# Optimization experiments

Measured on AMD Instinct MI355X. Metric: run time of the kernel, lower is better.

## Reference

```python
import jax, jax.numpy as jnp
import numpy as np

N = 50000   # nodes
R = 4       # relation groups
E = 800000  # nnz per relation adjacency
ED = 200000 # decoded edges
H = 128     # hidden_dim
L = 64      # latent_dim
DH = 64     # decoder_hidden_dim


def setup_inputs() -> dict:
    key = jax.random.key(0)
    ks = iter(jax.random.split(key, 64))
    def nrm(shape, scale=1.0):
        return jax.random.normal(next(ks), shape, dtype=jnp.float32) * scale
    inp = {}
    inp["x_process"] = nrm((N, 62))
    inp["x_file"] = nrm((N, 37))
    inp["x_network"] = nrm((N, 37))
    def lin(prefix, din, dout):
        s = 1.0 / np.sqrt(din)
        inp[prefix + "_Ws"] = nrm((dout, din), s)
        inp[prefix + "_bs"] = nrm((dout,), s)
        inp[prefix + "_Wr"] = nrm((R, dout, din), s)
        inp[prefix + "_br"] = nrm((R, dout), s)
    lin("p1", 62, H); lin("p2", H, L)
    lin("f1", 37, H); lin("f2", H, L)
    lin("n1", 37, H); lin("n2", H, L)
    inp["gate_W"] = nrm((3, L), 1.0 / np.sqrt(L))
    inp["gate_b"] = nrm((3,), 0.1)
    inp["dec_W1"] = nrm((DH, 4 * L), 1.0 / np.sqrt(4 * L))
    inp["dec_b1"] = nrm((DH,), 0.1)
    inp["dec_W2"] = nrm((1, DH), 1.0 / np.sqrt(DH))
    inp["dec_b2"] = nrm((1,), 0.1)
    inp["adj_rows"] = jax.random.randint(next(ks), (R, E), 0, N, dtype=jnp.int32)
    inp["adj_cols"] = jax.random.randint(next(ks), (R, E), 0, N, dtype=jnp.int32)
    inp["adj_vals"] = jax.random.uniform(next(ks), (R, E), dtype=jnp.float32) * 0.1
    inp["edge_src"] = jax.random.randint(next(ks), (ED,), 0, N, dtype=jnp.int32)
    inp["edge_dst"] = jax.random.randint(next(ks), (ED,), 0, N, dtype=jnp.int32)
    return inp


def reference(x_process, x_file, x_network,
              p1_Ws, p1_bs, p1_Wr, p1_br, p2_Ws, p2_bs, p2_Wr, p2_br,
              f1_Ws, f1_bs, f1_Wr, f1_br, f2_Ws, f2_bs, f2_Wr, f2_br,
              n1_Ws, n1_bs, n1_Wr, n1_br, n2_Ws, n2_bs, n2_Wr, n2_br,
              gate_W, gate_b, dec_W1, dec_b1, dec_W2, dec_b2,
              adj_rows, adj_cols, adj_vals, edge_src, edge_dst):
    def spmm(rows, cols, vals, x):  # A @ x, A in COO: out[row] += val * x[col]
        return jax.ops.segment_sum(vals[:, None] * x[cols], rows, num_segments=N)

    def rgcn_layer(x, Ws, bs, Wr, br):
        out = x @ Ws.T + bs  # self_linear
        for r in range(R):
            out = out + spmm(adj_rows[r], adj_cols[r], adj_vals[r], x) @ Wr[r].T + br[r]
        return out / float(R + 1)

    def encoder(x, W1s, b1s, W1r, b1r, W2s, b2s, W2r, b2r):
        h = jax.nn.relu(rgcn_layer(x, W1s, b1s, W1r, b1r))
        # dropout p=0.0 / eval mode -> identity
        return rgcn_layer(h, W2s, b2s, W2r, b2r)

    z_p = encoder(x_process, p1_Ws, p1_bs, p1_Wr, p1_br, p2_Ws, p2_bs, p2_Wr, p2_br)
    z_f = encoder(x_file, f1_Ws, f1_bs, f1_Wr, f1_br, f2_Ws, f2_bs, f2_Wr, f2_br)
    z_n = encoder(x_network, n1_Ws, n1_bs, n1_Wr, n1_br, n2_Ws, n2_bs, n2_Wr, n2_br)

    # gated multi-view fusion: three Linear(latent,1) gates -> softmax over views
    scores = jnp.stack([z_p @ gate_W[0] + gate_b[0],
                        z_f @ gate_W[1] + gate_b[1],
                        z_n @ gate_W[2] + gate_b[2]], axis=1)  # [N, 3]
    alpha = jax.nn.softmax(scores, axis=1)
    z = alpha[:, 0:1] * z_p + alpha[:, 1:2] * z_f + alpha[:, 2:3] * z_n  # [N, L]

    # mlp edge decoder
    zs = z[edge_src]
    zd = z[edge_dst]
    feats = jnp.concatenate([zs, zd, zs * zd, jnp.abs(zs - zd)], axis=1)  # [ED, 4L]
    hid = jax.nn.relu(feats @ dec_W1.T + dec_b1)
    logits = (hid @ dec_W2.T + dec_b2)[:, 0]  # [ED]
    return logits
```

## Files before the change

kernel.cpp:

```cpp
#include <hip/hip_runtime.h>

#define N_NODES 50000
#define R_REL   4
#define E_NNZ   800000
#define ED_EDGES 200000
#define H_DIM   128
#define L_DIM   64

#define RN_TOTAL (R_REL * N_NODES)
#define ETOT     (R_REL * E_NNZ)

#define EPB   8192
#define NB    391
#define RBK   196
#define KBK   (R_REL * RBK)
#define HTOT  (KBK * NB)
#define SCB   300
#define MAXB  6144

#define WS_RP    0u
#define WS_HIST  800256u
#define WS_BSUM  2026496u
#define WS_BIAS3 (WS_BSUM + 2048u)
#define WS_CV    2030592u
#define WS_TMP   27630720u
#define WS_XALL  53230720u
#define WS_SP    72430720u
#define WS_SF    122030720u
#define WS_SN    151630720u
#define WS_HPR   181230720u
#define WS_HN    WS_TMP
#define WS_HF    WS_SP
#define WS_YSP   WS_XALL
#define WS_YSF   (WS_SP + 25600000u)
#define WS_YRP   WS_SF
#define WS_YRF   WS_SN
#define WS_YSN   WS_HPR
#define WS_YRN   WS_HF
#define WS_Z     194030720u
#define WS_PART  WS_TMP

__device__ __forceinline__ ushort f2bf(float f) {
    unsigned u = __float_as_uint(f);
    unsigned r = (u + 0x7fffu + ((u >> 16) & 1u)) >> 16;
    return (ushort)r;
}
__device__ __forceinline__ float bf2f(ushort u) {
    return __uint_as_float(((unsigned)u) << 16);
}

__global__ void cast_xall_kernel(const float* __restrict__ xp, const float* __restrict__ xf,
                                 const float* __restrict__ xn, ushort* __restrict__ xall) {
    int i = blockIdx.x * 256 + threadIdx.x;
    if (i >= N_NODES * 192) return;
    int node = i / 192, k = i - node * 192;
    float v = 0.f;
    if (k < 62) v = xp[node * 62 + k];
    else if (k >= 64 && k < 138) {
        int j = k - 64, d = j >> 1;
        v = (j & 1) ? xn[node * 37 + d] : xf[node * 37 + d];
    }
    xall[i] = f2bf(v);
}

__global__ void radix_hist_kernel(const int* __restrict__ rows, int* __restrict__ H) {
    __shared__ int hist[KBK];
    int blk = blockIdx.x, t = threadIdx.x;
    for (int i = t; i < KBK; i += 256) hist[i] = 0;
    __syncthreads();
    int base = blk * EPB;
    #pragma unroll 1
    for (int i = 0; i < EPB / 256; i++) {
        int g = base + i * 256 + t;
        if (g < ETOT) {
            int r = g / E_NNZ;
            atomicAdd(&hist[r * RBK + (rows[g] >> 8)], 1);
        }
    }
    __syncthreads();
    for (int i = t; i < KBK; i += 256) H[i * NB + blk] = hist[i];
}

__global__ void scan_part_kernel(const int* __restrict__ H, int* __restrict__ bsum) {
    __shared__ int red[256];
    int base = blockIdx.x * 1024, t = threadIdx.x;
    int s = 0;
    #pragma unroll
    for (int i = 0; i < 4; i++) {
        int idx = base + i * 256 + t;
        if (idx < HTOT) s += H[idx];
    }
    red[t] = s; __syncthreads();
    for (int d = 128; d > 0; d >>= 1) {
        if (t < d) red[t] += red[t + d];
        __syncthreads();
    }
    if (t == 0) bsum[blockIdx.x] = red[0];
}

__global__ void scan_bsum_kernel(int* __restrict__ bsum, int* __restrict__ rp) {
    __shared__ int sh[512];
    int t = threadIdx.x;
    int v = (t < SCB) ? bsum[t] : 0;
    sh[t] = v; __syncthreads();
    for (int d = 1; d < 512; d <<= 1) {
        int u = (t >= d) ? sh[t - d] : 0;
        __syncthreads();
        sh[t] += u;
        __syncthreads();
    }
    if (t < SCB) bsum[t] = sh[t] - v;
    if (t == 0) rp[RN_TOTAL] = ETOT;
}

__global__ void scan_final_kernel(int* __restrict__ H, const int* __restrict__ bsum) {
    __shared__ int sh[256];
    int base = blockIdx.x * 1024, t = threadIdx.x;
    int c[4]; int s = 0;
    #pragma unroll
    for (int i = 0; i < 4; i++) {
        int idx = base + t * 4 + i;
        c[i] = (idx < HTOT) ? H[idx] : 0;
        s += c[i];
    }
    sh[t] = s; __syncthreads();
    for (int d = 1; d < 256; d <<= 1) {
        int u = (t >= d) ? sh[t - d] : 0;
        __syncthreads();
        sh[t] += u;
        __syncthreads();
    }
    int off = bsum[blockIdx.x] + sh[t] - s;
    #pragma unroll
    for (int i = 0; i < 4; i++) {
        int idx = base + t * 4 + i;
        if (idx < HTOT) H[idx] = off;
        off += c[i];
    }
}

__global__ void radix_scatter_kernel(const int* __restrict__ rows, const int* __restrict__ cols,
                                     const float* __restrict__ vals, const int* __restrict__ H,
                                     int2* __restrict__ tmp) {
    __shared__ int cur[KBK];
    int blk = blockIdx.x, t = threadIdx.x;
    for (int i = t; i < KBK; i += 256) cur[i] = H[i * NB + blk];
    __syncthreads();
    int base = blk * EPB;
    #pragma unroll 1
    for (int i = 0; i < EPB / 256; i++) {
        int g = base + i * 256 + t;
        if (g < ETOT) {
            int r = g / E_NNZ;
            int row = rows[g];
            int b = r * RBK + (row >> 8);
            int p = atomicAdd(&cur[b], 1);
            tmp[p] = make_int2(cols[g] | ((row & 255) << 16), __float_as_int(vals[g]));
        }
    }
}

__launch_bounds__(256)
__global__ void bucket_sort_kernel(const int2* __restrict__ tmp, const int* __restrict__ H,
                                   int* __restrict__ rp, int2* __restrict__ cse) {
    __shared__ int hist[256];
    __shared__ int sc[256];
    __shared__ int cur[256];
    __shared__ int2 eb[MAXB];
    int b = blockIdx.x, t = threadIdx.x;
    int start = H[b * NB];
    int end = (b == KBK - 1) ? ETOT : H[(b + 1) * NB];
    int cnt = end - start;
    bool useLds = (cnt <= MAXB);
    hist[t] = 0;
    __syncthreads();
    for (int i = t; i < cnt; i += 256) {
        int2 e = tmp[start + i];
        if (useLds) eb[i] = e;
        atomicAdd(&hist[(e.x >> 16) & 255], 1);
    }
    __syncthreads();
    sc[t] = hist[t]; __syncthreads();
    for (int d = 1; d < 256; d <<= 1) {
        int v = (t >= d) ? sc[t - d] : 0;
        __syncthreads();
        sc[t] += v;
        __syncthreads();
    }
    int pref = sc[t] - hist[t];
    int r = b / RBK, rh = b - r * RBK;
    int grow = rh * 256 + t;
    if (grow < N_NODES) rp[r * N_NODES + grow] = start + pref;
    cur[t] = start + pref;
    __syncthreads();
    for (int i = t; i < cnt; i += 256) {
        int2 e = useLds ? eb[i] : tmp[start + i];
        int rl = (e.x >> 16) & 255;
        int p = atomicAdd(&cur[rl], 1);
        cse[p] = make_int2(e.x & 0xFFFF, e.y);
    }
}

__global__ void spmm1_all_kernel(const ushort* __restrict__ xall,
                                 const int* __restrict__ rp, const int2* __restrict__ cse,
                                 float* __restrict__ Sp, float* __restrict__ Sf,
                                 float* __restrict__ Sn) {
    int wave = threadIdx.x >> 6, lane = threadIdx.x & 63;
    int row = blockIdx.x * 4 + wave;
    if (row >= N_NODES) return;
    int h = lane >> 5, j = lane & 31;
    unsigned d0 = 2u * (unsigned)j;
    unsigned po = d0;
    unsigned fo = 64u + 2u * d0;
    for (int r = 0; r < R_REL; r++) {
        int e0 = rp[r * N_NODES + row], e1 = rp[r * N_NODES + row + 1];
        float ap0 = 0.f, ap1 = 0.f, af0 = 0.f, af1 = 0.f, an0 = 0.f, an1 = 0.f;
        int e = e0;
        for (; e + 8 <= e1; e += 8) {
            int2 qA = cse[e + h],     qB = cse[e + 2 + h];
            int2 qC = cse[e + 4 + h], qD = cse[e + 6 + h];
            unsigned bA = (unsigned)qA.x * 192u, bB = (unsigned)qB.x * 192u;
            unsigned bC = (unsigned)qC.x * 192u, bD = (unsigned)qD.x * 192u;
            ushort2 pA = *(const ushort2*)(xall + bA + po);
            ushort2 pB = *(const ushort2*)(xall + bB + po);
            ushort2 pC = *(const ushort2*)(xall + bC + po);
            ushort2 pD = *(const ushort2*)(xall + bD + po);
            ushort4 uA = *(const ushort4*)(xall + bA + fo);
            ushort4 uB = *(const ushort4*)(xall + bB + fo);
            ushort4 uC = *(const ushort4*)(xall + bC + fo);
            ushort4 uD = *(const ushort4*)(xall + bD + fo);
            float vA = __int_as_float(qA.y), vB = __int_as_float(qB.y);
            float vC = __int_as_float(qC.y), vD = __int_as_float(qD.y);
            ap0 += vA * bf2f(pA.x) + vB * bf2f(pB.x) + vC * bf2f(pC.x) + vD * bf2f(pD.x);
            ap1 += vA * bf2f(pA.y) + vB * bf2f(pB.y) + vC * bf2f(pC.y) + vD * bf2f(pD.y);
            af0 += vA * bf2f(uA.x) + vB * bf2f(uB.x) + vC * bf2f(uC.x) + vD * bf2f(uD.x);
            an0 += vA * bf2f(uA.y) + vB * bf2f(uB.y) + vC * bf2f(uC.y) + vD * bf2f(uD.y);
            af1 += vA * bf2f(uA.z) + vB * bf2f(uB.z) + vC * bf2f(uC.z) + vD * bf2f(uD.z);
            an1 += vA * bf2f(uA.w) + vB * bf2f(uB.w) + vC * bf2f(uC.w) + vD * bf2f(uD.w);
        }
        for (; e < e1; e += 2) {
            int idx = e + h;
            int2 q = cse[idx < e1 ? idx : e1 - 1];
            float v = (idx < e1) ? __int_as_float(q.y) : 0.f;
            unsigned b = (unsigned)q.x * 192u;
            ushort2 p = *(const ushort2*)(xall + b + po);
            ushort4 u = *(const ushort4*)(xall + b + fo);
            ap0 += v * bf2f(p.x); ap1 += v * bf2f(p.y);
            af0 += v * bf2f(u.x); an0 += v * bf2f(u.y);
            af1 += v * bf2f(u.z); an1 += v * bf2f(u.w);
        }
        ap0 += __shfl_xor(ap0, 32); ap1 += __shfl_xor(ap1, 32);
        af0 += __shfl_xor(af0, 32); af1 += __shfl_xor(af1, 32);
        an0 += __shfl_xor(an0, 32); an1 += __shfl_xor(an1, 32);
        if (h == 0) {
            int d = (int)d0;
            if (d < 62) *(float2*)(Sp + row * 248 + r * 62 + d) = make_float2(ap0, ap1);
            float* sfp = Sf + row * 148 + r * 37;
            float* snp = Sn + row * 148 + r * 37;
            if (d < 37) { sfp[d] = af0; snp[d] = an0; }
            if (d < 36) { sfp[d + 1] = af1; snp[d + 1] = an1; }
        }
    }
}

__launch_bounds__(256)
__global__ void gemm1_kernel(const float* __restrict__ x, const float* __restrict__ S,
                             const float* __restrict__ Ws, const float* __restrict__ bs,
                             const float* __restrict__ Wr, const float* __restrict__ br,
                             float* __restrict__ h, int din) {
    __shared__ float sA[64 * 63];
    __shared__ float sW[62 * 132];
    int t = threadIdx.x;
    int i0 = blockIdx.x * 64;
    int rg = t >> 5, cg = t & 31;
    float acc[8][4] = {};
    for (int s = 0; s < 5; s++) {
        const float* Aptr; int astride;
        if (s == 0) { Aptr = x; astride = din; }
        else        { Aptr = S + (s - 1) * din; astride = 4 * din; }
        const float* Wp = (s == 0) ? Ws : (Wr + (s - 1) * H_DIM * din);
        __syncthreads();
        for (int idx = t; idx < 64 * din; idx += 256) {
            int rr = idx / din, k = idx - rr * din;
            int grow = i0 + rr;
            sA[rr * 63 + k] = (grow < N_NODES) ? Aptr[grow * astride + k] : 0.f;
        }
        for (int idx = t; idx < H_DIM * din; idx += 256) {
            int j = idx / din, k = idx - j * din;
            sW[k * 132 + j] = Wp[j * din + k];
        }
        __syncthreads();
        for (int k = 0; k < din; k++) {
            float a[8];
            #pragma unroll
            for (int rr = 0; rr < 8; rr++) a[rr] = sA[(rg * 8 + rr) * 63 + k];
            float4 w = *(const float4*)&sW[k * 132 + cg * 4];
            #pragma unroll
            for (int rr = 0; rr < 8; rr++) {
                acc[rr][0] += a[rr] * w.x; acc[rr][1] += a[rr] * w.y;
                acc[rr][2] += a[rr] * w.z; acc[rr][3] += a[rr] * w.w;
            }
        }
    }
    int j0 = cg * 4;
    float btot[4];
    #pragma unroll
    for (int cc = 0; cc < 4; cc++) {
        float b = bs[j0 + cc];
        #pragma unroll
        for (int r = 0; r < R_REL; r++) b += br[r * H_DIM + j0 + cc];
        btot[cc] = b;
    }
    #pragma unroll
    for (int rr = 0; rr < 8; rr++) {
        int grow = i0 + rg * 8 + rr;
        if (grow < N_NODES) {
            float4 o;
            o.x = fmaxf((acc[rr][0] + btot[0]) * 0.2f, 0.f);
            o.y = fmaxf((acc[rr][1] + btot[1]) * 0.2f, 0.f);
            o.z = fmaxf((acc[rr][2] + btot[2]) * 0.2f, 0.f);
            o.w = fmaxf((acc[rr][3] + btot[3]) * 0.2f, 0.f);
            *(float4*)&h[grow * H_DIM + j0] = o;
        }
    }
}

__launch_bounds__(256)
__global__ void gemm2_kernel(const float* __restrict__ h, const float* __restrict__ Ws2,
                             const float* __restrict__ Wr2, float* __restrict__ Yself,
                             ushort* __restrict__ Yrel) {
    __shared__ float sA[128 * 65];
    __shared__ float sW[64 * 68];
    int t = threadIdx.x;
    int i0 = blockIdx.x * 128;
    int ct = blockIdx.y;
    int rg = t >> 4, cg = t & 15;
    const float* Wp = (ct == 0) ? Ws2 : (Wr2 + (ct - 1) * 64 * H_DIM);
    float acc[8][4] = {};
    for (int kc = 0; kc < 2; kc++) {
        __syncthreads();
        for (int idx = t; idx < 128 * 64; idx += 256) {
            int rr = idx >> 6, k = idx & 63;
            int grow = i0 + rr;
            sA[rr * 65 + k] = (grow < N_NODES) ? h[grow * H_DIM + kc * 64 + k] : 0.f;
        }
        for (int idx = t; idx < 64 * 64; idx += 256) {
            int j = idx >> 6, k = idx & 63;
            sW[k * 68 + j] = Wp[j * H_DIM + kc * 64 + k];
        }
        __syncthreads();
        for (int k = 0; k < 64; k++) {
            float a[8];
            #pragma unroll
            for (int rr = 0; rr < 8; rr++) a[rr] = sA[(rg * 8 + rr) * 65 + k];
            float4 w = *(const float4*)&sW[k * 68 + cg * 4];
            #pragma unroll
            for (int rr = 0; rr < 8; rr++) {
                acc[rr][0] += a[rr] * w.x; acc[rr][1] += a[rr] * w.y;
                acc[rr][2] += a[rr] * w.z; acc[rr][3] += a[rr] * w.w;
            }
        }
    }
    #pragma unroll
    for (int rr = 0; rr < 8; rr++) {
        int grow = i0 + rg * 8 + rr;
        if (grow < N_NODES) {
            if (ct == 0) {
                float4 o = make_float4(acc[rr][0], acc[rr][1], acc[rr][2], acc[rr][3]);
                *(float4*)&Yself[(size_t)grow * 64 + cg * 4] = o;
            } else {
                ushort4 o;
                o.x = f2bf(acc[rr][0]); o.y = f2bf(acc[rr][1]);
                o.z = f2bf(acc[rr][2]); o.w = f2bf(acc[rr][3]);
                *(ushort4*)&Yrel[(size_t)grow * 256 + (ct - 1) * 64 + cg * 4] = o;
            }
        }
    }
}

__global__ void bias_prep_kernel(const float* __restrict__ pbs, const float* __restrict__ pbr,
                                 const float* __restrict__ fbs, const float* __restrict__ fbr,
                                 const float* __restrict__ nbs, const float* __restrict__ nbr,
                                 float* __restrict__ bias3) {
    int t = threadIdx.x;
    if (t >= 192) return;
    int view = t >> 6, d = t & 63;
    const float* bs = (view == 0) ? pbs : (view == 1) ? fbs : nbs;
    const float* br = (view == 0) ? pbr : (view == 1) ? fbr : nbr;
    float b = bs[d];
    #pragma unroll
    for (int r = 0; r < R_REL; r++) b += br[r * 64 + d];
    bias3[t] = b;
}

__global__ void spmm2z_all_kernel(const float* __restrict__ Ysp, const ushort* __restrict__ Yrp,
                                  const float* __restrict__ Ysf, const ushort* __restrict__ Yrf,
                                  const float* __restrict__ Ysn, const ushort* __restrict__ Yrn,
                                  const int* __restrict__ rp, const int2* __restrict__ cse,
                                  const float* __restrict__ bias3,
                                  const float* __restrict__ gW, const float* __restrict__ gb,
                                  float* __restrict__ z) {
    int wave = threadIdx.x >> 6, lane = threadIdx.x & 63;
    int row = blockIdx.x * 4 + wave;
    if (row >= N_NODES) return;
    int h = lane >> 5, j = lane & 31;
    unsigned d0 = 2u * (unsigned)j;
    float aP0 = 0.f, aP1 = 0.f, aF0 = 0.f, aF1 = 0.f, aN0 = 0.f, aN1 = 0.f;
    for (int r = 0; r < R_REL; r++) {
        int e0 = rp[r * N_NODES + row], e1 = rp[r * N_NODES + row + 1];
        unsigned ofs = (unsigned)(r * 64) + d0;
        int e = e0;
        for (; e + 8 <= e1; e += 8) {
            int2 qA = cse[e + h],     qB = cse[e + 2 + h];
            int2 qC = cse[e + 4 + h], qD = cse[e + 6 + h];
            unsigned oA = (unsigned)qA.x * 256u + ofs;
            unsigned oB = (unsigned)qB.x * 256u + ofs;
            unsigned oC = (unsigned)qC.x * 256u + ofs;
            unsigned oD = (unsigned)qD.x * 256u + ofs;
            ushort2 pA = *(const ushort2*)(Yrp + oA), pB = *(const ushort2*)(Yrp + oB);
            ushort2 pC = *(const ushort2*)(Yrp + oC), pD = *(const ushort2*)(Yrp + oD);
            ushort2 fA = *(const ushort2*)(Yrf + oA), fB = *(const ushort2*)(Yrf + oB);
            ushort2 fC = *(const ushort2*)(Yrf + oC), fD = *(const ushort2*)(Yrf + oD);
            ushort2 nA = *(const ushort2*)(Yrn + oA), nB = *(const ushort2*)(Yrn + oB);
            ushort2 nC = *(const ushort2*)(Yrn + oC), nD = *(const ushort2*)(Yrn + oD);
            float vA = __int_as_float(qA.y), vB = __int_as_float(qB.y);
            float vC = __int_as_float(qC.y), vD = __int_as_float(qD.y);
            aP0 += vA * bf2f(pA.x) + vB * bf2f(pB.x) + vC * bf2f(pC.x) + vD * bf2f(pD.x);
            aP1 += vA * bf2f(pA.y) + vB * bf2f(pB.y) + vC * bf2f(pC.y) + vD * bf2f(pD.y);
            aF0 += vA * bf2f(fA.x) + vB * bf2f(fB.x) + vC * bf2f(fC.x) + vD * bf2f(fD.x);
            aF1 += vA * bf2f(fA.y) + vB * bf2f(fB.y) + vC * bf2f(fC.y) + vD * bf2f(fD.y);
            aN0 += vA * bf2f(nA.x) + vB * bf2f(nB.x) + vC * bf2f(nC.x) + vD * bf2f(nD.x);
            aN1 += vA * bf2f(nA.y) + vB * bf2f(nB.y) + vC * bf2f(nC.y) + vD * bf2f(nD.y);
        }
        for (; e < e1; e += 2) {
            int idx = e + h;
            int2 q = cse[idx < e1 ? idx : e1 - 1];
            float v = (idx < e1) ? __int_as_float(q.y) : 0.f;
            unsigned o = (unsigned)q.x * 256u + ofs;
            ushort2 p = *(const ushort2*)(Yrp + o);
            ushort2 f = *(const ushort2*)(Yrf + o);
            ushort2 n = *(const ushort2*)(Yrn + o);
            aP0 += v * bf2f(p.x); aP1 += v * bf2f(p.y);
            aF0 += v * bf2f(f.x); aF1 += v * bf2f(f.y);
            aN0 += v * bf2f(n.x); aN1 += v * bf2f(n.y);
        }
    }
    aP0 += __shfl_xor(aP0, 32); aP1 += __shfl_xor(aP1, 32);
    aF0 += __shfl_xor(aF0, 32); aF1 += __shfl_xor(aF1, 32);
    aN0 += __shfl_xor(aN0, 32); aN1 += __shfl_xor(aN1, 32);
    size_t rb = (size_t)row * 64 + d0;
    float2 ysp = *(const float2*)(Ysp + rb);
    float2 ysf = *(const float2*)(Ysf + rb);
    float2 ysn = *(const float2*)(Ysn + rb);
    aP0 = (aP0 + ysp.x + bias3[d0]) * 0.2f;
    aP1 = (aP1 + ysp.y + bias3[d0 + 1]) * 0.2f;
    aF0 = (aF0 + ysf.x + bias3[64 + d0]) * 0.2f;
    aF1 = (aF1 + ysf.y + bias3[64 + d0 + 1]) * 0.2f;
    aN0 = (aN0 + ysn.x + bias3[128 + d0]) * 0.2f;
    aN1 = (aN1 + ysn.y + bias3[128 + d0 + 1]) * 0.2f;
    float sp = aP0 * gW[d0] + aP1 * gW[d0 + 1];
    float sf = aF0 * gW[64 + d0] + aF1 * gW[64 + d0 + 1];
    float sn = aN0 * gW[128 + d0] + aN1 * gW[128 + d0 + 1];
    #pragma unroll
    for (int d = 16; d >= 1; d >>= 1) {
        sp += __shfl_xor(sp, d);
        sf += __shfl_xor(sf, d);
        sn += __shfl_xor(sn, d);
    }
    sp += gb[0]; sf += gb[1]; sn += gb[2];
    float m = fmaxf(sp, fmaxf(sf, sn));
    float ep = __expf(sp - m), ef = __expf(sf - m), en = __expf(sn - m);
    float inv = 1.f / (ep + ef + en);
    if (h == 0) {
        float2 zo;
        zo.x = (ep * aP0 + ef * aF0 + en * aN0) * inv;
        zo.y = (ep * aP1 + ef * aF1 + en * aN1) * inv;
        *(float2*)(z + rb) = zo;
    }
}

__launch_bounds__(256)
__global__ void decoder5_kernel(const float* __restrict__ z, const int* __restrict__ esrc,
                                const int* __restrict__ edst, const float* __restrict__ w1,
                                const float* __restrict__ b1, const float* __restrict__ w2,
                                float* __restrict__ part) {
    __shared__ float sW1[8192];
    int t = threadIdx.x;
    int jh = blockIdx.y;
    const float* w1h = w1 + jh * 32 * 256;
    for (int i = t; i < 2048; i += 256)
        ((float4*)sW1)[i] = ((const float4*)w1h)[i];
    __syncthreads();
    int e1 = blockIdx.x * 512 + t;
    int e2 = e1 + 256;
    bool v2 = e2 < ED_EDGES;
    if (e1 >= ED_EDGES) return;
    int s1 = esrc[e1], d1 = edst[e1];
    int s2 = v2 ? esrc[e2] : s1;
    int d2 = v2 ? edst[e2] : d1;
    const float4* zs1 = (const float4*)(z + (size_t)s1 * 64);
    const float4* zd1 = (const float4*)(z + (size_t)d1 * 64);
    const float4* zs2 = (const float4*)(z + (size_t)s2 * 64);
    const float4* zd2 = (const float4*)(z + (size_t)d2 * 64);
    float hid1[32], hid2[32];
    #pragma unroll
    for (int j = 0; j < 32; j++) { hid1[j] = 0.f; hid2[j] = 0.f; }
    #pragma unroll 1
    for (int kc = 0; kc < 16; kc++) {
        float4 a1 = zs1[kc], b1v4 = zd1[kc];
        float4 a2 = zs2[kc], b2v4 = zd2[kc];
        float4 p1, q1, p2, q2;
        p1.x = a1.x * b1v4.x; q1.x = fabsf(a1.x - b1v4.x);
        p1.y = a1.y * b1v4.y; q1.y = fabsf(a1.y - b1v4.y);
        p1.z = a1.z * b1v4.z; q1.z = fabsf(a1.z - b1v4.z);
        p1.w = a1.w * b1v4.w; q1.w = fabsf(a1.w - b1v4.w);
        p2.x = a2.x * b2v4.x; q2.x = fabsf(a2.x - b2v4.x);
        p2.y = a2.y * b2v4.y; q2.y = fabsf(a2.y - b2v4.y);
        p2.z = a2.z * b2v4.z; q2.z = fabsf(a2.z - b2v4.z);
        p2.w = a2.w * b2v4.w; q2.w = fabsf(a2.w - b2v4.w);
        const float* wb0 = sW1 + kc * 4;
        #pragma unroll
        for (int j = 0; j < 32; j++) {
            const float* wr = wb0 + j * 256;
            float4 wa = *(const float4*)(wr);
            float4 wbv = *(const float4*)(wr + 64);
            float4 wc = *(const float4*)(wr + 128);
            float4 wd = *(const float4*)(wr + 192);
            hid1[j] += a1.x * wa.x + a1.y * wa.y + a1.z * wa.z + a1.w * wa.w
                     + b1v4.x * wbv.x + b1v4.y * wbv.y + b1v4.z * wbv.z + b1v4.w * wbv.w
                     + p1.x * wc.x + p1.y * wc.y + p1.z * wc.z + p1.w * wc.w
                     + q1.x * wd.x + q1.y * wd.y + q1.z * wd.z + q1.w * wd.w;
            hid2[j] += a2.x * wa.x + a2.y * wa.y + a2.z * wa.z + a2.w * wa.w
                     + b2v4.x * wbv.x + b2v4.y * wbv.y + b2v4.z * wbv.z + b2v4.w * wbv.w
                     + p2.x * wc.x + p2.y * wc.y + p2.z * wc.z + p2.w * wc.w
                     + q2.x * wd.x + q2.y * wd.y + q2.z * wd.z + q2.w * wd.w;
        }
    }
    float lg1 = 0.f, lg2 = 0.f;
    #pragma unroll
    for (int j = 0; j < 32; j++) {
        int gj = jh * 32 + j;
        float bj = b1[gj], wj = w2[gj];
        lg1 += fmaxf(hid1[j] + bj, 0.f) * wj;
        lg2 += fmaxf(hid2[j] + bj, 0.f) * wj;
    }
    part[(size_t)jh * ED_EDGES + e1] = lg1;
    if (v2) part[(size_t)jh * ED_EDGES + e2] = lg2;
}

__global__ void dec_combine_kernel(const float* __restrict__ part, const float* __restrict__ b2,
                                   float* __restrict__ out) {
    int e = blockIdx.x * 256 + threadIdx.x;
    if (e < ED_EDGES) out[e] = part[e] + part[ED_EDGES + e] + b2[0];
}

extern "C" void kernel_launch(void* const* d_in, const int* in_sizes, int n_in,
                              void* d_out, int out_size, void* d_ws, size_t ws_size,
                              hipStream_t stream) {
    const float* x_p = (const float*)d_in[0];
    const float* x_f = (const float*)d_in[1];
    const float* x_n = (const float*)d_in[2];
    const float* p1_Ws = (const float*)d_in[3];  const float* p1_bs = (const float*)d_in[4];
    const float* p1_Wr = (const float*)d_in[5];  const float* p1_br = (const float*)d_in[6];
    const float* p2_Ws = (const float*)d_in[7];  const float* p2_bs = (const float*)d_in[8];
    const float* p2_Wr = (const float*)d_in[9];  const float* p2_br = (const float*)d_in[10];
    const float* f1_Ws = (const float*)d_in[11]; const float* f1_bs = (const float*)d_in[12];
    const float* f1_Wr = (const float*)d_in[13]; const float* f1_br = (const float*)d_in[14];
    const float* f2_Ws = (const float*)d_in[15]; const float* f2_bs = (const float*)d_in[16];
    const float* f2_Wr = (const float*)d_in[17]; const float* f2_br = (const float*)d_in[18];
    const float* n1_Ws = (const float*)d_in[19]; const float* n1_bs = (const float*)d_in[20];
    const float* n1_Wr = (const float*)d_in[21]; const float* n1_br = (const float*)d_in[22];
    const float* n2_Ws = (const float*)d_in[23]; const float* n2_bs = (const float*)d_in[24];
    const float* n2_Wr = (const float*)d_in[25]; const float* n2_br = (const float*)d_in[26];
    const float* gate_W = (const float*)d_in[27]; const float* gate_b = (const float*)d_in[28];
    const float* dec_W1 = (const float*)d_in[29]; const float* dec_b1 = (const float*)d_in[30];
    const float* dec_W2 = (const float*)d_in[31]; const float* dec_b2 = (const float*)d_in[32];
    const int*   adj_rows = (const int*)d_in[33];
    const int*   adj_cols = (const int*)d_in[34];
    const float* adj_vals = (const float*)d_in[35];
    const int*   edge_src = (const int*)d_in[36];
    const int*   edge_dst = (const int*)d_in[37];

    char* ws = (char*)d_ws;
    int*    rp   = (int*)(ws + WS_RP);
    int*    H    = (int*)(ws + WS_HIST);
    int*    bsum = (int*)(ws + WS_BSUM);
    float*  bias3 = (float*)(ws + WS_BIAS3);
    int2*   cse  = (int2*)(ws + WS_CV);
    int2*   tmp  = (int2*)(ws + WS_TMP);
    ushort* xall = (ushort*)(ws + WS_XALL);
    float*  S_p = (float*)(ws + WS_SP);
    float*  S_f = (float*)(ws + WS_SF);
    float*  S_n = (float*)(ws + WS_SN);
    float*  h_p = (float*)(ws + WS_HPR);
    float*  h_f = (float*)(ws + WS_HF);
    float*  h_n = (float*)(ws + WS_HN);
    float*  Ys_p = (float*)(ws + WS_YSP);  ushort* Yr_p = (ushort*)(ws + WS_YRP);
    float*  Ys_f = (float*)(ws + WS_YSF);  ushort* Yr_f = (ushort*)(ws + WS_YRF);
    float*  Ys_n = (float*)(ws + WS_YSN);  ushort* Yr_n = (ushort*)(ws + WS_YRN);
    float*  z    = (float*)(ws + WS_Z);
    float*  part = (float*)(ws + WS_PART);
    float*  out  = (float*)d_out;

    cast_xall_kernel<<<(N_NODES * 192 + 255) / 256, 256, 0, stream>>>(x_p, x_f, x_n, xall);

    radix_hist_kernel<<<NB, 256, 0, stream>>>(adj_rows, H);
    scan_part_kernel<<<SCB, 256, 0, stream>>>(H, bsum);
    scan_bsum_kernel<<<1, 512, 0, stream>>>(bsum, rp);
    scan_final_kernel<<<SCB, 256, 0, stream>>>(H, bsum);
    radix_scatter_kernel<<<NB, 256, 0, stream>>>(adj_rows, adj_cols, adj_vals, H, tmp);
    bucket_sort_kernel<<<KBK, 256, 0, stream>>>(tmp, H, rp, cse);

    spmm1_all_kernel<<<N_NODES / 4, 256, 0, stream>>>(xall, rp, cse, S_p, S_f, S_n);

    int g1 = (N_NODES + 63) / 64;
    gemm1_kernel<<<g1, 256, 0, stream>>>(x_p, S_p, p1_Ws, p1_bs, p1_Wr, p1_br, h_p, 62);
    gemm1_kernel<<<g1, 256, 0, stream>>>(x_f, S_f, f1_Ws, f1_bs, f1_Wr, f1_br, h_f, 37);
    gemm1_kernel<<<g1, 256, 0, stream>>>(x_n, S_n, n1_Ws, n1_bs, n1_Wr, n1_br, h_n, 37);

    dim3 g2((N_NODES + 127) / 128, 5);
    gemm2_kernel<<<g2, 256, 0, stream>>>(h_p, p2_Ws, p2_Wr, Ys_p, Yr_p);
    gemm2_kernel<<<g2, 256, 0, stream>>>(h_f, f2_Ws, f2_Wr, Ys_f, Yr_f);
    gemm2_kernel<<<g2, 256, 0, stream>>>(h_n, n2_Ws, n2_Wr, Ys_n, Yr_n);

    bias_prep_kernel<<<1, 192, 0, stream>>>(p2_bs, p2_br, f2_bs, f2_br, n2_bs, n2_br, bias3);
    spmm2z_all_kernel<<<N_NODES / 4, 256, 0, stream>>>(
        Ys_p, Yr_p, Ys_f, Yr_f, Ys_n, Yr_n, rp, cse, bias3, gate_W, gate_b, z);

    dim3 gd((ED_EDGES + 511) / 512, 2);
    decoder5_kernel<<<gd, 256, 0, stream>>>(
        z, edge_src, edge_dst, dec_W1, dec_b1, dec_W2, part);
    dec_combine_kernel<<<(ED_EDGES + 255) / 256, 256, 0, stream>>>(part, dec_b2, out);
}
```

Baseline: 1.401 ms.

## Software-pipeline edge index loads across relations in both SpMM kernels

Both SpMM gather kernels now walk all four relation segments of a row as one continuous stream of 8-edge chunks. The index/value loads for the next chunk are issued before the current chunk's accumulation, with a sched_barrier to keep that order. The old per-relation scalar tail loop is replaced by masked full chunks, so rows with few edges per relation avoid serial remainder iterations. This adds control-flow and register pressure for the relation-switch logic and per-relation flushes, and launch bounds are added.

```diff
diff --git a/kernel.cpp b/kernel.cpp
--- a/kernel.cpp
+++ b/kernel.cpp
@@ -201,6 +201,7 @@
     }
 }
 
+__launch_bounds__(256)
 __global__ void spmm1_all_kernel(const ushort* __restrict__ xall,
                                  const int* __restrict__ rp, const int2* __restrict__ cse,
                                  float* __restrict__ Sp, float* __restrict__ Sf,
@@ -212,55 +213,83 @@
     unsigned d0 = 2u * (unsigned)j;
     unsigned po = d0;
     unsigned fo = 64u + 2u * d0;
-    for (int r = 0; r < R_REL; r++) {
-        int e0 = rp[r * N_NODES + row], e1 = rp[r * N_NODES + row + 1];
-        float ap0 = 0.f, ap1 = 0.f, af0 = 0.f, af1 = 0.f, an0 = 0.f, an1 = 0.f;
-        int e = e0;
-        for (; e + 8 <= e1; e += 8) {
-            int2 qA = cse[e + h],     qB = cse[e + 2 + h];
-            int2 qC = cse[e + 4 + h], qD = cse[e + 6 + h];
-            unsigned bA = (unsigned)qA.x * 192u, bB = (unsigned)qB.x * 192u;
-            unsigned bC = (unsigned)qC.x * 192u, bD = (unsigned)qD.x * 192u;
-            ushort2 pA = *(const ushort2*)(xall + bA + po);
-            ushort2 pB = *(const ushort2*)(xall + bB + po);
-            ushort2 pC = *(const ushort2*)(xall + bC + po);
-            ushort2 pD = *(const ushort2*)(xall + bD + po);
-            ushort4 uA = *(const ushort4*)(xall + bA + fo);
-            ushort4 uB = *(const ushort4*)(xall + bB + fo);
-            ushort4 uC = *(const ushort4*)(xall + bC + fo);
-            ushort4 uD = *(const ushort4*)(xall + bD + fo);
-            float vA = __int_as_float(qA.y), vB = __int_as_float(qB.y);
-            float vC = __int_as_float(qC.y), vD = __int_as_float(qD.y);
-            ap0 += vA * bf2f(pA.x) + vB * bf2f(pB.x) + vC * bf2f(pC.x) + vD * bf2f(pD.x);
-            ap1 += vA * bf2f(pA.y) + vB * bf2f(pB.y) + vC * bf2f(pC.y) + vD * bf2f(pD.y);
-            af0 += vA * bf2f(uA.x) + vB * bf2f(uB.x) + vC * bf2f(uC.x) + vD * bf2f(uD.x);
-            an0 += vA * bf2f(uA.y) + vB * bf2f(uB.y) + vC * bf2f(uC.y) + vD * bf2f(uD.y);
-            af1 += vA * bf2f(uA.z) + vB * bf2f(uB.z) + vC * bf2f(uC.z) + vD * bf2f(uD.z);
-            an1 += vA * bf2f(uA.w) + vB * bf2f(uB.w) + vC * bf2f(uC.w) + vD * bf2f(uD.w);
-        }
-        for (; e < e1; e += 2) {
-            int idx = e + h;
-            int2 q = cse[idx < e1 ? idx : e1 - 1];
-            float v = (idx < e1) ? __int_as_float(q.y) : 0.f;
-            unsigned b = (unsigned)q.x * 192u;
-            ushort2 p = *(const ushort2*)(xall + b + po);
-            ushort4 u = *(const ushort4*)(xall + b + fo);
-            ap0 += v * bf2f(p.x); ap1 += v * bf2f(p.y);
-            af0 += v * bf2f(u.x); an0 += v * bf2f(u.y);
-            af1 += v * bf2f(u.z); an1 += v * bf2f(u.w);
-        }
-        ap0 += __shfl_xor(ap0, 32); ap1 += __shfl_xor(ap1, 32);
-        af0 += __shfl_xor(af0, 32); af1 += __shfl_xor(af1, 32);
-        an0 += __shfl_xor(an0, 32); an1 += __shfl_xor(an1, 32);
-        if (h == 0) {
-            int d = (int)d0;
-            if (d < 62) *(float2*)(Sp + row * 248 + r * 62 + d) = make_float2(ap0, ap1);
-            float* sfp = Sf + row * 148 + r * 37;
-            float* snp = Sn + row * 148 + r * 37;
-            if (d < 37) { sfp[d] = af0; snp[d] = an0; }
-            if (d < 36) { sfp[d + 1] = af1; snp[d + 1] = an1; }
-        }
-    }
+
+    int e, lim, rpos;
+    int nsA, ntA, nsB, ntB, nsC, ntC;
+    e   = rp[row];               lim = rp[row + 1];
+    nsA = rp[N_NODES + row];     ntA = rp[N_NODES + row + 1];
+    nsB = rp[2 * N_NODES + row]; ntB = rp[2 * N_NODES + row + 1];
+    nsC = rp[3 * N_NODES + row]; ntC = rp[3 * N_NODES + row + 1];
+    rpos = 0;
+    while (e >= lim && rpos < 3) {
+        rpos++; e = nsA; lim = ntA;
+        nsA = nsB; ntA = ntB; nsB = nsC; ntB = ntC;
+    }
+    bool vCur = (e < lim);
+    float ap0 = 0.f, ap1 = 0.f, af0 = 0.f, af1 = 0.f, an0 = 0.f, an1 = 0.f;
+    int rcur = 0;
+
+    int2 qA, qB, qC, qD;
+    if (vCur) {
+        int lm = lim - 1;
+        qA = cse[min(e + h, lm)];     qB = cse[min(e + 2 + h, lm)];
+        qC = cse[min(e + 4 + h, lm)]; qD = cse[min(e + 6 + h, lm)];
+    }
+
+#define SPMM1_FLUSH(RR) {                                                       \
+        ap0 += __shfl_xor(ap0, 32); ap1 += __shfl_xor(ap1, 32);                 \
+        af0 += __shfl_xor(af0, 32); af1 += __shfl_xor(af1, 32);                 \
+        an0 += __shfl_xor(an0, 32); an1 += __shfl_xor(an1, 32);                 \
+        if (h == 0) {                                                           \
+            int d = (int)d0;                                                    \
+            if (d < 62) *(float2*)(Sp + row * 248 + (RR) * 62 + d) =            \
+                            make_float2(ap0, ap1);                              \
+            float* sfp = Sf + row * 148 + (RR) * 37;                            \
+            float* snp = Sn + row * 148 + (RR) * 37;                            \
+            if (d < 37) { sfp[d] = af0; snp[d] = an0; }                         \
+            if (d < 36) { sfp[d + 1] = af1; snp[d + 1] = an1; }                 \
+        }                                                                       \
+        ap0 = 0.f; ap1 = 0.f; af0 = 0.f; af1 = 0.f; an0 = 0.f; an1 = 0.f; }
+
+    while (vCur) {
+        int rChunk = rpos;
+        float vA = (e + h     < lim) ? __int_as_float(qA.y) : 0.f;
+        float vB = (e + 2 + h < lim) ? __int_as_float(qB.y) : 0.f;
+        float vC = (e + 4 + h < lim) ? __int_as_float(qC.y) : 0.f;
+        float vD = (e + 6 + h < lim) ? __int_as_float(qD.y) : 0.f;
+        unsigned bA = (unsigned)qA.x * 192u, bB = (unsigned)qB.x * 192u;
+        unsigned bC = (unsigned)qC.x * 192u, bD = (unsigned)qD.x * 192u;
+        ushort2 pA = *(const ushort2*)(xall + bA + po);
+        ushort2 pB = *(const ushort2*)(xall + bB + po);
+        ushort2 pC = *(const ushort2*)(xall + bC + po);
+        ushort2 pD = *(const ushort2*)(xall + bD + po);
+        ushort4 uA = *(const ushort4*)(xall + bA + fo);
+        ushort4 uB = *(const ushort4*)(xall + bB + fo);
+        ushort4 uC = *(const ushort4*)(xall + bC + fo);
+        ushort4 uD = *(const ushort4*)(xall + bD + fo);
+        e += 8;
+        while (e >= lim && rpos < 3) {
+            rpos++; e = nsA; lim = ntA;
+            nsA = nsB; ntA = ntB; nsB = nsC; ntB = ntC;
+        }
+        bool vNext = (e < lim);
+        if (vNext) {
+            int lm = lim - 1;
+            qA = cse[min(e + h, lm)];     qB = cse[min(e + 2 + h, lm)];
+            qC = cse[min(e + 4 + h, lm)]; qD = cse[min(e + 6 + h, lm)];
+        }
+        __builtin_amdgcn_sched_barrier(0);
+        while (rcur < rChunk) { SPMM1_FLUSH(rcur); rcur++; }
+        ap0 += vA * bf2f(pA.x) + vB * bf2f(pB.x) + vC * bf2f(pC.x) + vD * bf2f(pD.x);
+        ap1 += vA * bf2f(pA.y) + vB * bf2f(pB.y) + vC * bf2f(pC.y) + vD * bf2f(pD.y);
+        af0 += vA * bf2f(uA.x) + vB * bf2f(uB.x) + vC * bf2f(uC.x) + vD * bf2f(uD.x);
+        an0 += vA * bf2f(uA.y) + vB * bf2f(uB.y) + vC * bf2f(uC.y) + vD * bf2f(uD.y);
+        af1 += vA * bf2f(uA.z) + vB * bf2f(uB.z) + vC * bf2f(uC.z) + vD * bf2f(uD.z);
+        an1 += vA * bf2f(uA.w) + vB * bf2f(uB.w) + vC * bf2f(uC.w) + vD * bf2f(uD.w);
+        vCur = vNext;
+    }
+    while (rcur < 4) { SPMM1_FLUSH(rcur); rcur++; }
+#undef SPMM1_FLUSH
 }
 
 __launch_bounds__(256)
@@ -393,6 +422,7 @@
     bias3[t] = b;
 }
 
+__launch_bounds__(256)
 __global__ void spmm2z_all_kernel(const float* __restrict__ Ysp, const ushort* __restrict__ Yrp,
                                   const float* __restrict__ Ysf, const ushort* __restrict__ Yrf,
                                   const float* __restrict__ Ysn, const ushort* __restrict__ Yrn,
@@ -405,45 +435,62 @@
     if (row >= N_NODES) return;
     int h = lane >> 5, j = lane & 31;
     unsigned d0 = 2u * (unsigned)j;
+
+    int e, lim, rpos;
+    int nsA, ntA, nsB, ntB, nsC, ntC;
+    e   = rp[row];               lim = rp[row + 1];
+    nsA = rp[N_NODES + row];     ntA = rp[N_NODES + row + 1];
+    nsB = rp[2 * N_NODES + row]; ntB = rp[2 * N_NODES + row + 1];
+    nsC = rp[3 * N_NODES + row]; ntC = rp[3 * N_NODES + row + 1];
+    rpos = 0;
+    while (e >= lim && rpos < 3) {
+        rpos++; e = nsA; lim = ntA;
+        nsA = nsB; ntA = ntB; nsB = nsC; ntB = ntC;
+    }
+    bool vCur = (e < lim);
     float aP0 = 0.f, aP1 = 0.f, aF0 = 0.f, aF1 = 0.f, aN0 = 0.f, aN1 = 0.f;
-    for (int r = 0; r < R_REL; r++) {
-        int e0 = rp[r * N_NODES + row], e1 = rp[r * N_NODES + row + 1];
-        unsigned ofs = (unsigned)(r * 64) + d0;
-        int e = e0;
-        for (; e + 8 <= e1; e += 8) {
-            int2 qA = cse[e + h],     qB = cse[e + 2 + h];
-            int2 qC = cse[e + 4 + h], qD = cse[e + 6 + h];
-            unsigned oA = (unsigned)qA.x * 256u + ofs;
-            unsigned oB = (unsigned)qB.x * 256u + ofs;
-            unsigned oC = (unsigned)qC.x * 256u + ofs;
-            unsigned oD = (unsigned)qD.x * 256u + ofs;
-            ushort2 pA = *(const ushort2*)(Yrp + oA), pB = *(const ushort2*)(Yrp + oB);
-            ushort2 pC = *(const ushort2*)(Yrp + oC), pD = *(const ushort2*)(Yrp + oD);
-            ushort2 fA = *(const ushort2*)(Yrf + oA), fB = *(const ushort2*)(Yrf + oB);
-            ushort2 fC = *(const ushort2*)(Yrf + oC), fD = *(const ushort2*)(Yrf + oD);
-            ushort2 nA = *(const ushort2*)(Yrn + oA), nB = *(const ushort2*)(Yrn + oB);
-            ushort2 nC = *(const ushort2*)(Yrn + oC), nD = *(const ushort2*)(Yrn + oD);
-            float vA = __int_as_float(qA.y), vB = __int_as_float(qB.y);
-            float vC = __int_as_float(qC.y), vD = __int_as_float(qD.y);
-            aP0 += vA * bf2f(pA.x) + vB * bf2f(pB.x) + vC * bf2f(pC.x) + vD * bf2f(pD.x);
-            aP1 += vA * bf2f(pA.y) + vB * bf2f(pB.y) + vC * bf2f(pC.y) + vD * bf2f(pD.y);
-            aF0 += vA * bf2f(fA.x) + vB * bf2f(fB.x) + vC * bf2f(fC.x) + vD * bf2f(fD.x);
-            aF1 += vA * bf2f(fA.y) + vB * bf2f(fB.y) + vC * bf2f(fC.y) + vD * bf2f(fD.y);
-            aN0 += vA * bf2f(nA.x) + vB * bf2f(nB.x) + vC * bf2f(nC.x) + vD * bf2f(nD.x);
-            aN1 += vA * bf2f(nA.y) + vB * bf2f(nB.y) + vC * bf2f(nC.y) + vD * bf2f(nD.y);
-        }
-        for (; e < e1; e += 2) {
-            int idx = e + h;
-            int2 q = cse[idx < e1 ? idx : e1 - 1];
-            float v = (idx < e1) ? __int_as_float(q.y) : 0.f;
-            unsigned o = (unsigned)q.x * 256u + ofs;
-            ushort2 p = *(const ushort2*)(Yrp + o);
-            ushort2 f = *(const ushort2*)(Yrf + o);
-            ushort2 n = *(const ushort2*)(Yrn + o);
-            aP0 += v * bf2f(p.x); aP1 += v * bf2f(p.y);
-            aF0 += v * bf2f(f.x); aF1 += v * bf2f(f.y);
-            aN0 += v * bf2f(n.x); aN1 += v * bf2f(n.y);
-        }
+
+    int2 qA, qB, qC, qD;
+    if (vCur) {
+        int lm = lim - 1;
+        qA = cse[min(e + h, lm)];     qB = cse[min(e + 2 + h, lm)];
+        qC = cse[min(e + 4 + h, lm)]; qD = cse[min(e + 6 + h, lm)];
+    }
+    while (vCur) {
+        unsigned ofs = ((unsigned)rpos << 6) + d0;
+        float vA = (e + h     < lim) ? __int_as_float(qA.y) : 0.f;
+        float vB = (e + 2 + h < lim) ? __int_as_float(qB.y) : 0.f;
+        float vC = (e + 4 + h < lim) ? __int_as_float(qC.y) : 0.f;
+        float vD = (e + 6 + h < lim) ? __int_as_float(qD.y) : 0.f;
+        unsigned oA = (unsigned)qA.x * 256u + ofs;
+        unsigned oB = (unsigned)qB.x * 256u + ofs;
+        unsigned oC = (unsigned)qC.x * 256u + ofs;
+        unsigned oD = (unsigned)qD.x * 256u + ofs;
+        ushort2 pA = *(const ushort2*)(Yrp + oA), pB = *(const ushort2*)(Yrp + oB);
+        ushort2 pC = *(const ushort2*)(Yrp + oC), pD = *(const ushort2*)(Yrp + oD);
+        ushort2 fA = *(const ushort2*)(Yrf + oA), fB = *(const ushort2*)(Yrf + oB);
+        ushort2 fC = *(const ushort2*)(Yrf + oC), fD = *(const ushort2*)(Yrf + oD);
+        ushort2 nA = *(const ushort2*)(Yrn + oA), nB = *(const ushort2*)(Yrn + oB);
+        ushort2 nC = *(const ushort2*)(Yrn + oC), nD = *(const ushort2*)(Yrn + oD);
+        e += 8;
+        while (e >= lim && rpos < 3) {
+            rpos++; e = nsA; lim = ntA;
+            nsA = nsB; ntA = ntB; nsB = nsC; ntB = ntC;
+        }
+        bool vNext = (e < lim);
+        if (vNext) {
+            int lm = lim - 1;
+            qA = cse[min(e + h, lm)];     qB = cse[min(e + 2 + h, lm)];
+            qC = cse[min(e + 4 + h, lm)]; qD = cse[min(e + 6 + h, lm)];
+        }
+        __builtin_amdgcn_sched_barrier(0);
+        aP0 += vA * bf2f(pA.x) + vB * bf2f(pB.x) + vC * bf2f(pC.x) + vD * bf2f(pD.x);
+        aP1 += vA * bf2f(pA.y) + vB * bf2f(pB.y) + vC * bf2f(pC.y) + vD * bf2f(pD.y);
+        aF0 += vA * bf2f(fA.x) + vB * bf2f(fB.x) + vC * bf2f(fC.x) + vD * bf2f(fD.x);
+        aF1 += vA * bf2f(fA.y) + vB * bf2f(fB.y) + vC * bf2f(fC.y) + vD * bf2f(fD.y);
+        aN0 += vA * bf2f(nA.x) + vB * bf2f(nB.x) + vC * bf2f(nC.x) + vD * bf2f(nD.x);
+        aN1 += vA * bf2f(nA.y) + vB * bf2f(nB.y) + vC * bf2f(nC.y) + vD * bf2f(nD.y);
+        vCur = vNext;
     }
     aP0 += __shfl_xor(aP0, 32); aP1 += __shfl_xor(aP1, 32);
     aF0 += __shfl_xor(aF0, 32); aF1 += __shfl_xor(aF1, 32);
```

After: 1.399 ms. No clear change (-0.2%).

## Interleave per-view relation outputs into one buffer and fuse decoder into single kernel

Applied to the files above, without the earlier changes.

The gemm2 outputs for all three views are now written interleaved into one bf16 buffer laid out [node][rel][view][64]. The gather in spmm2z then reads the p/f/n values for a neighbor from one contiguous 384-byte region instead of three separate arrays, which improves cache-line locality on the random gathers. The decoder is also rewritten so each thread computes all 64 hidden units for a single edge, with the full W1 held in 64KB of shared memory. This removes the partial-sum buffer and the combine kernel, but it raises register pressure (64 accumulators) and halves the per-thread edge reuse of the weight loads.

```diff
diff --git a/kernel.cpp b/kernel.cpp
--- a/kernel.cpp
+++ b/kernel.cpp
@@ -21,24 +21,21 @@
 #define WS_RP    0u
 #define WS_HIST  800256u
 #define WS_BSUM  2026496u
-#define WS_BIAS3 (WS_BSUM + 2048u)
+#define WS_BIAS3 2028544u
 #define WS_CV    2030592u
+#define WS_YALL  27630720u
 #define WS_TMP   27630720u
-#define WS_XALL  53230720u
-#define WS_SP    72430720u
-#define WS_SF    122030720u
-#define WS_SN    151630720u
-#define WS_HPR   181230720u
-#define WS_HN    WS_TMP
-#define WS_HF    WS_SP
-#define WS_YSP   WS_XALL
-#define WS_YSF   (WS_SP + 25600000u)
-#define WS_YRP   WS_SF
-#define WS_YRF   WS_SN
-#define WS_YSN   WS_HPR
-#define WS_YRN   WS_HF
-#define WS_Z     194030720u
-#define WS_PART  WS_TMP
+#define WS_SF    53230720u
+#define WS_SN    82830720u
+#define WS_XALL  112430720u
+#define WS_YSP   112430720u
+#define WS_SP    131630720u
+#define WS_HF    131630720u
+#define WS_YSN   131630720u
+#define WS_HN    157230720u
+#define WS_HPR   188001536u
+#define WS_YSF   188001536u
+#define WS_Z     200801536u
 
 __device__ __forceinline__ ushort f2bf(float f) {
     unsigned u = __float_as_uint(f);
@@ -328,7 +325,7 @@
 __launch_bounds__(256)
 __global__ void gemm2_kernel(const float* __restrict__ h, const float* __restrict__ Ws2,
                              const float* __restrict__ Wr2, float* __restrict__ Yself,
-                             ushort* __restrict__ Yrel) {
+                             ushort* __restrict__ Yall, int view) {
     __shared__ float sA[128 * 65];
     __shared__ float sW[64 * 68];
     int t = threadIdx.x;
@@ -372,7 +369,7 @@
                 ushort4 o;
                 o.x = f2bf(acc[rr][0]); o.y = f2bf(acc[rr][1]);
                 o.z = f2bf(acc[rr][2]); o.w = f2bf(acc[rr][3]);
-                *(ushort4*)&Yrel[(size_t)grow * 256 + (ct - 1) * 64 + cg * 4] = o;
+                *(ushort4*)&Yall[(size_t)grow * 768 + (ct - 1) * 192 + view * 64 + cg * 4] = o;
             }
         }
     }
@@ -393,9 +390,11 @@
     bias3[t] = b;
 }
 
-__global__ void spmm2z_all_kernel(const float* __restrict__ Ysp, const ushort* __restrict__ Yrp,
-                                  const float* __restrict__ Ysf, const ushort* __restrict__ Yrf,
-                                  const float* __restrict__ Ysn, const ushort* __restrict__ Yrn,
+__launch_bounds__(256)
+__global__ void spmm2z_all_kernel(const float* __restrict__ Ysp,
+                                  const float* __restrict__ Ysf,
+                                  const float* __restrict__ Ysn,
+                                  const ushort* __restrict__ Yall,
                                   const int* __restrict__ rp, const int2* __restrict__ cse,
                                   const float* __restrict__ bias3,
                                   const float* __restrict__ gW, const float* __restrict__ gb,
@@ -408,21 +407,27 @@
     float aP0 = 0.f, aP1 = 0.f, aF0 = 0.f, aF1 = 0.f, aN0 = 0.f, aN1 = 0.f;
     for (int r = 0; r < R_REL; r++) {
         int e0 = rp[r * N_NODES + row], e1 = rp[r * N_NODES + row + 1];
-        unsigned ofs = (unsigned)(r * 64) + d0;
+        unsigned ofs = (unsigned)(r * 192) + d0;
         int e = e0;
         for (; e + 8 <= e1; e += 8) {
             int2 qA = cse[e + h],     qB = cse[e + 2 + h];
             int2 qC = cse[e + 4 + h], qD = cse[e + 6 + h];
-            unsigned oA = (unsigned)qA.x * 256u + ofs;
-            unsigned oB = (unsigned)qB.x * 256u + ofs;
-            unsigned oC = (unsigned)qC.x * 256u + ofs;
-            unsigned oD = (unsigned)qD.x * 256u + ofs;
-            ushort2 pA = *(const ushort2*)(Yrp + oA), pB = *(const ushort2*)(Yrp + oB);
-            ushort2 pC = *(const ushort2*)(Yrp + oC), pD = *(const ushort2*)(Yrp + oD);
-            ushort2 fA = *(const ushort2*)(Yrf + oA), fB = *(const ushort2*)(Yrf + oB);
-            ushort2 fC = *(const ushort2*)(Yrf + oC), fD = *(const ushort2*)(Yrf + oD);
-            ushort2 nA = *(const ushort2*)(Yrn + oA), nB = *(const ushort2*)(Yrn + oB);
-            ushort2 nC = *(const ushort2*)(Yrn + oC), nD = *(const ushort2*)(Yrn + oD);
+            unsigned oA = (unsigned)qA.x * 768u + ofs;
+            unsigned oB = (unsigned)qB.x * 768u + ofs;
+            unsigned oC = (unsigned)qC.x * 768u + ofs;
+            unsigned oD = (unsigned)qD.x * 768u + ofs;
+            ushort2 pA = *(const ushort2*)(Yall + oA);
+            ushort2 fA = *(const ushort2*)(Yall + oA + 64);
+            ushort2 nA = *(const ushort2*)(Yall + oA + 128);
+            ushort2 pB = *(const ushort2*)(Yall + oB);
+            ushort2 fB = *(const ushort2*)(Yall + oB + 64);
+            ushort2 nB = *(const ushort2*)(Yall + oB + 128);
+            ushort2 pC = *(const ushort2*)(Yall + oC);
+            ushort2 fC = *(const ushort2*)(Yall + oC + 64);
+            ushort2 nC = *(const ushort2*)(Yall + oC + 128);
+            ushort2 pD = *(const ushort2*)(Yall + oD);
+            ushort2 fD = *(const ushort2*)(Yall + oD + 64);
+            ushort2 nD = *(const ushort2*)(Yall + oD + 128);
             float vA = __int_as_float(qA.y), vB = __int_as_float(qB.y);
             float vC = __int_as_float(qC.y), vD = __int_as_float(qD.y);
             aP0 += vA * bf2f(pA.x) + vB * bf2f(pB.x) + vC * bf2f(pC.x) + vD * bf2f(pD.x);
@@ -436,10 +441,10 @@
             int idx = e + h;
             int2 q = cse[idx < e1 ? idx : e1 - 1];
             float v = (idx < e1) ? __int_as_float(q.y) : 0.f;
-            unsigned o = (unsigned)q.x * 256u + ofs;
-            ushort2 p = *(const ushort2*)(Yrp + o);
-            ushort2 f = *(const ushort2*)(Yrf + o);
-            ushort2 n = *(const ushort2*)(Yrn + o);
+            unsigned o = (unsigned)q.x * 768u + ofs;
+            ushort2 p = *(const ushort2*)(Yall + o);
+            ushort2 f = *(const ushort2*)(Yall + o + 64);
+            ushort2 n = *(const ushort2*)(Yall + o + 128);
             aP0 += v * bf2f(p.x); aP1 += v * bf2f(p.y);
             aF0 += v * bf2f(f.x); aF1 += v * bf2f(f.y);
             aN0 += v * bf2f(n.x); aN1 += v * bf2f(n.y);
@@ -479,79 +484,51 @@
     }
 }
 
-__launch_bounds__(256)
-__global__ void decoder5_kernel(const float* __restrict__ z, const int* __restrict__ esrc,
+__launch_bounds__(512)
+__global__ void decoder6_kernel(const float* __restrict__ z, const int* __restrict__ esrc,
                                 const int* __restrict__ edst, const float* __restrict__ w1,
                                 const float* __restrict__ b1, const float* __restrict__ w2,
-                                float* __restrict__ part) {
-    __shared__ float sW1[8192];
+                                const float* __restrict__ b2, float* __restrict__ out) {
+    __shared__ float sW1[16384];
     int t = threadIdx.x;
-    int jh = blockIdx.y;
-    const float* w1h = w1 + jh * 32 * 256;
-    for (int i = t; i < 2048; i += 256)
-        ((float4*)sW1)[i] = ((const float4*)w1h)[i];
+    for (int i = t; i < 4096; i += 512)
+        ((float4*)sW1)[i] = ((const float4*)w1)[i];
     __syncthreads();
-    int e1 = blockIdx.x * 512 + t;
-    int e2 = e1 + 256;
-    bool v2 = e2 < ED_EDGES;
-    if (e1 >= ED_EDGES) return;
-    int s1 = esrc[e1], d1 = edst[e1];
-    int s2 = v2 ? esrc[e2] : s1;
-    int d2 = v2 ? edst[e2] : d1;
-    const float4* zs1 = (const float4*)(z + (size_t)s1 * 64);
-    const float4* zd1 = (const float4*)(z + (size_t)d1 * 64);
-    const float4* zs2 = (const float4*)(z + (size_t)s2 * 64);
-    const float4* zd2 = (const float4*)(z + (size_t)d2 * 64);
-    float hid1[32], hid2[32];
-    #pragma unroll
-    for (int j = 0; j < 32; j++) { hid1[j] = 0.f; hid2[j] = 0.f; }
+    int e = blockIdx.x * 512 + t;
+    if (e >= ED_EDGES) return;
+    int s = esrc[e], d = edst[e];
+    const float4* zs = (const float4*)(z + (size_t)s * 64);
+    const float4* zd = (const float4*)(z + (size_t)d * 64);
+    float hid[64];
+    #pragma unroll
+    for (int j = 0; j < 64; j++) hid[j] = 0.f;
     #pragma unroll 1
     for (int kc = 0; kc < 16; kc++) {
-        float4 a1 = zs1[kc], b1v4 = zd1[kc];
-        float4 a2 = zs2[kc], b2v4 = zd2[kc];
-        float4 p1, q1, p2, q2;
-        p1.x = a1.x * b1v4.x; q1.x = fabsf(a1.x - b1v4.x);
-        p1.y = a1.y * b1v4.y; q1.y = fabsf(a1.y - b1v4.y);
-        p1.z = a1.z * b1v4.z; q1.z = fabsf(a1.z - b1v4.z);
-        p1.w = a1.w * b1v4.w; q1.w = fabsf(a1.w - b1v4.w);
-        p2.x = a2.x * b2v4.x; q2.x = fabsf(a2.x - b2v4.x);
-        p2.y = a2.y * b2v4.y; q2.y = fabsf(a2.y - b2v4.y);
-        p2.z = a2.z * b2v4.z; q2.z = fabsf(a2.z - b2v4.z);
-        p2.w = a2.w * b2v4.w; q2.w = fabsf(a2.w - b2v4.w);
+        float4 a = zs[kc], b = zd[kc];
+        float4 p, q;
+        p.x = a.x * b.x; q.x = fabsf(a.x - b.x);
+        p.y = a.y * b.y; q.y = fabsf(a.y - b.y);
+        p.z = a.z * b.z; q.z = fabsf(a.z - b.z);
+        p.w = a.w * b.w; q.w = fabsf(a.w - b.w);
         const float* wb0 = sW1 + kc * 4;
         #pragma unroll
-        for (int j = 0; j < 32; j++) {
+        for (int j = 0; j < 64; j++) {
             const float* wr = wb0 + j * 256;
             float4 wa = *(const float4*)(wr);
             float4 wbv = *(const float4*)(wr + 64);
             float4 wc = *(const float4*)(wr + 128);
             float4 wd = *(const float4*)(wr + 192);
-            hid1[j] += a1.x * wa.x + a1.y * wa.y + a1.z * wa.z + a1.w * wa.w
-                     + b1v4.x * wbv.x + b1v4.y * wbv.y + b1v4.z * wbv.z + b1v4.w * wbv.w
-                     + p1.x * wc.x + p1.y * wc.y + p1.z * wc.z + p1.w * wc.w
-                     + q1.x * wd.x + q1.y * wd.y + q1.z * wd.z + q1.w * wd.w;
-            hid2[j] += a2.x * wa.x + a2.y * wa.y + a2.z * wa.z + a2.w * wa.w
-                     + b2v4.x * wbv.x + b2v4.y * wbv.y + b2v4.z * wbv.z + b2v4.w * wbv.w
-                     + p2.x * wc.x + p2.y * wc.y + p2.z * wc.z + p2.w * wc.w
-                     + q2.x * wd.x + q2.y * wd.y + q2.z * wd.z + q2.w * wd.w;
-        }
-    }
-    float lg1 = 0.f, lg2 = 0.f;
-    #pragma unroll
-    for (int j = 0; j < 32; j++) {
-        int gj = jh * 32 + j;
-        float bj = b1[gj], wj = w2[gj];
-        lg1 += fmaxf(hid1[j] + bj, 0.f) * wj;
-        lg2 += fmaxf(hid2[j] + bj, 0.f) * wj;
-    }
-    part[(size_t)jh * ED_EDGES + e1] = lg1;
-    if (v2) part[(size_t)jh * ED_EDGES + e2] = lg2;
-}
-
-__global__ void dec_combine_kernel(const float* __restrict__ part, const float* __restrict__ b2,
-                                   float* __restrict__ out) {
-    int e = blockIdx.x * 256 + threadIdx.x;
-    if (e < ED_EDGES) out[e] = part[e] + part[ED_EDGES + e] + b2[0];
+            hid[j] += a.x * wa.x + a.y * wa.y + a.z * wa.z + a.w * wa.w
+                    + b.x * wbv.x + b.y * wbv.y + b.z * wbv.z + b.w * wbv.w
+                    + p.x * wc.x + p.y * wc.y + p.z * wc.z + p.w * wc.w
+                    + q.x * wd.x + q.y * wd.y + q.z * wd.z + q.w * wd.w;
+        }
+    }
+    float lg = b2[0];
+    #pragma unroll
+    for (int j = 0; j < 64; j++)
+        lg += fmaxf(hid[j] + b1[j], 0.f) * w2[j];
+    out[e] = lg;
 }
 
 extern "C" void kernel_launch(void* const* d_in, const int* in_sizes, int n_in,
@@ -589,17 +566,17 @@
     int2*   cse  = (int2*)(ws + WS_CV);
     int2*   tmp  = (int2*)(ws + WS_TMP);
     ushort* xall = (ushort*)(ws + WS_XALL);
+    ushort* Yall = (ushort*)(ws + WS_YALL);
     float*  S_p = (float*)(ws + WS_SP);
     float*  S_f = (float*)(ws + WS_SF);
     float*  S_n = (float*)(ws + WS_SN);
     float*  h_p = (float*)(ws + WS_HPR);
     float*  h_f = (float*)(ws + WS_HF);
     float*  h_n = (float*)(ws + WS_HN);
-    float*  Ys_p = (float*)(ws + WS_YSP);  ushort* Yr_p = (ushort*)(ws + WS_YRP);
-    float*  Ys_f = (float*)(ws + WS_YSF);  ushort* Yr_f = (ushort*)(ws + WS_YRF);
-    float*  Ys_n = (float*)(ws + WS_YSN);  ushort* Yr_n = (ushort*)(ws + WS_YRN);
+    float*  Ys_p = (float*)(ws + WS_YSP);
+    float*  Ys_f = (float*)(ws + WS_YSF);
+    float*  Ys_n = (float*)(ws + WS_YSN);
     float*  z    = (float*)(ws + WS_Z);
-    float*  part = (float*)(ws + WS_PART);
     float*  out  = (float*)d_out;
 
     cast_xall_kernel<<<(N_NODES * 192 + 255) / 256, 256, 0, stream>>>(x_p, x_f, x_n, xall);
@@ -619,16 +596,14 @@
     gemm1_kernel<<<g1, 256, 0, stream>>>(x_n, S_n, n1_Ws, n1_bs, n1_Wr, n1_br, h_n, 37);
 
     dim3 g2((N_NODES + 127) / 128, 5);
-    gemm2_kernel<<<g2, 256, 0, stream>>>(h_p, p2_Ws, p2_Wr, Ys_p, Yr_p);
-    gemm2_kernel<<<g2, 256, 0, stream>>>(h_f, f2_Ws, f2_Wr, Ys_f, Yr_f);
-    gemm2_kernel<<<g2, 256, 0, stream>>>(h_n, n2_Ws, n2_Wr, Ys_n, Yr_n);
+    gemm2_kernel<<<g2, 256, 0, stream>>>(h_p, p2_Ws, p2_Wr, Ys_p, Yall, 0);
+    gemm2_kernel<<<g2, 256, 0, stream>>>(h_f, f2_Ws, f2_Wr, Ys_f, Yall, 1);
+    gemm2_kernel<<<g2, 256, 0, stream>>>(h_n, n2_Ws, n2_Wr, Ys_n, Yall, 2);
 
     bias_prep_kernel<<<1, 192, 0, stream>>>(p2_bs, p2_br, f2_bs, f2_br, n2_bs, n2_br, bias3);
     spmm2z_all_kernel<<<N_NODES / 4, 256, 0, stream>>>(
-        Ys_p, Yr_p, Ys_f, Yr_f, Ys_n, Yr_n, rp, cse, bias3, gate_W, gate_b, z);
-
-    dim3 gd((ED_EDGES + 511) / 512, 2);
-    decoder5_kernel<<<gd, 256, 0, stream>>>(
-        z, edge_src, edge_dst, dec_W1, dec_b1, dec_W2, part);
-    dec_combine_kernel<<<(ED_EDGES + 255) / 256, 256, 0, stream>>>(part, dec_b2, out);
-}
+        Ys_p, Ys_f, Ys_n, Yall, rp, cse, bias3, gate_W, gate_b, z);
+
+    decoder6_kernel<<<(ED_EDGES + 511) / 512, 512, 0, stream>>>(
+        z, edge_src, edge_dst, dec_W1, dec_b1, dec_W2, dec_b2, out);
+}
```

Measured after the change: 1.436 ms. 2.5% more time.
